# Kernel tuning notes

Hardware: AMD Instinct MI355X
Metric: run time of the kernel (lower is better)

## Reference

```python
import jax, jax.numpy as jnp
import numpy as np

NEG_SLOPE = 0.2


def setup_inputs() -> dict:
    key = jax.random.key(0)
    k1, k2, k3 = jax.random.split(key, 3)
    bs, n_agents, input_dim = 32, 512, 128
    n_heads, hidden_dim = 8, 64
    h = jax.random.normal(k1, (bs, n_agents, input_dim), dtype=jnp.float32)
    # Linear(input_dim, n_heads*hidden_dim, bias=False), stored as [in, out]
    W = jax.random.normal(k2, (input_dim, n_heads * hidden_dim), dtype=jnp.float32) * (1.0 / np.sqrt(input_dim))
    # xavier_uniform with gain=1.414 on shape (1, n_heads, 2*hidden_dim)
    fan = n_heads + 2 * hidden_dim
    bound = 1.414 * np.sqrt(6.0 / fan)
    att_a = jax.random.uniform(k3, (1, n_heads, 2 * hidden_dim), dtype=jnp.float32,
                               minval=-bound, maxval=bound)
    return {"h": h, "W": W, "att_a": att_a}


def reference(h, W, att_a):
    bs, n_agents, _ = h.shape
    n_heads = att_a.shape[1]
    hidden_dim = att_a.shape[2] // 2
    # h_prime: [bs, n_heads, n_agents, hidden_dim]
    h_prime = (h @ W).reshape(bs, n_agents, n_heads, hidden_dim).transpose(0, 2, 1, 3)
    # Additive score decomposes exactly: (a1.h_i + a2.h_j) == sum(cat(h_i,h_j)*a)
    a_src = att_a[0, :, :hidden_dim]   # [n_heads, hidden_dim]
    a_dst = att_a[0, :, hidden_dim:]   # [n_heads, hidden_dim]
    e_src = jnp.einsum('bhnd,hd->bhn', h_prime, a_src)  # score contribution of node i (row)
    e_dst = jnp.einsum('bhnd,hd->bhn', h_prime, a_dst)  # contribution of node j (col)
    e = e_src[:, :, :, None] + e_dst[:, :, None, :]     # [bs, n_heads, n, n]
    e = jnp.where(e >= 0, e, NEG_SLOPE * e)             # leaky_relu(0.2)
    attention = jax.nn.softmax(e, axis=-1)
    h_new = jnp.einsum('bhnm,bhmd->bhnd', attention, h_prime)
    return jax.nn.elu(h_new)
```

## Files before the change

### kernel.cpp

```cpp
#include <hip/hip_runtime.h>

#define BS 32
#define NA 512
#define ID 128
#define NH 8
#define HD 64
#define NHD 512
#define NEG 0.2f
#define NC 32
#define CH 16
#define NW 8
#define BPAD 136

typedef short bf16x8 __attribute__((ext_vector_type(8)));
typedef float f32x4 __attribute__((ext_vector_type(4)));

__device__ inline unsigned f2bf_bits(float x) {
  unsigned u = __float_as_uint(x);
  return (u + 0x7FFFu + ((u >> 16) & 1u)) >> 16;
}

__device__ inline void split8(const float4& x, const float4& y,
                              bf16x8& hi, bf16x8& lo) {
  float f[8] = {x.x, x.y, x.z, x.w, y.x, y.y, y.z, y.w};
  #pragma unroll
  for (int j = 0; j < 8; ++j) {
    unsigned hb = f2bf_bits(f[j]);
    float r = f[j] - __uint_as_float(hb << 16);
    unsigned lb = f2bf_bits(r);
    hi[j] = (short)hb;
    lo[j] = (short)lb;
  }
}

__global__ __launch_bounds__(256, 4) void k1_mfma(
    const float* __restrict__ h, const float* __restrict__ W,
    const float* __restrict__ att, float* __restrict__ io,
    float* __restrict__ sG, float* __restrict__ tG) {
  __shared__ unsigned short Bhi[64 * BPAD];
  __shared__ unsigned short Blo[64 * BPAD];

  int blk = blockIdx.x;
  int mt = blk >> 3;
  int n0 = (blk & 7) * 64;
  int m0 = mt * 128;
  int b = mt >> 2;
  int nbase = (mt & 3) * 128;
  int head = n0 >> 6;
  int t = threadIdx.x;
  int lane = t & 63, w = t >> 6;
  int q = lane >> 4, ml = lane & 15;

  {
    int c = t & 63, kq = t >> 6;
    const float* wsrc = W + (size_t)kq * 32 * NHD + n0 + c;
    #pragma unroll 4
    for (int kk = 0; kk < 32; ++kk) {
      int k = kq * 32 + kk;
      float x = wsrc[(size_t)kk * NHD];
      unsigned hb = f2bf_bits(x);
      float r = x - __uint_as_float(hb << 16);
      Bhi[c * BPAD + k] = (unsigned short)hb;
      Blo[c * BPAD + k] = (unsigned short)f2bf_bits(r);
    }
  }
  __syncthreads();

  f32x4 acc[2][4];
  #pragma unroll
  for (int mf = 0; mf < 2; ++mf)
    #pragma unroll
    for (int nf = 0; nf < 4; ++nf)
      acc[mf][nf] = (f32x4){0.f, 0.f, 0.f, 0.f};

  const float* A0 = h + (size_t)(m0 + w * 32 + ml) * ID;

  #pragma unroll
  for (int ks = 0; ks < 4; ++ks) {
    int ko = ks * 32 + q * 8;
    bf16x8 ah[2], al[2];
    #pragma unroll
    for (int mf = 0; mf < 2; ++mf) {
      const float* ap = A0 + mf * 16 * ID + ko;
      float4 f0 = *(const float4*)ap;
      float4 f1 = *(const float4*)(ap + 4);
      split8(f0, f1, ah[mf], al[mf]);
    }
    #pragma unroll
    for (int nf = 0; nf < 4; ++nf) {
      int bo = (nf * 16 + ml) * BPAD + ko;
      bf16x8 bh = *(const bf16x8*)&Bhi[bo];
      bf16x8 bl = *(const bf16x8*)&Blo[bo];
      #pragma unroll
      for (int mf = 0; mf < 2; ++mf) {
        acc[mf][nf] = __builtin_amdgcn_mfma_f32_16x16x32_bf16(ah[mf], bh, acc[mf][nf], 0, 0, 0);
        acc[mf][nf] = __builtin_amdgcn_mfma_f32_16x16x32_bf16(ah[mf], bl, acc[mf][nf], 0, 0, 0);
        acc[mf][nf] = __builtin_amdgcn_mfma_f32_16x16x32_bf16(al[mf], bh, acc[mf][nf], 0, 0, 0);
      }
    }
  }

  {
    float* ob = io + (((size_t)b * NH + head) * NA + nbase + w * 32) * HD + ml;
    #pragma unroll
    for (int mf = 0; mf < 2; ++mf)
      #pragma unroll
      for (int nf = 0; nf < 4; ++nf)
        #pragma unroll
        for (int r = 0; r < 4; ++r)
          ob[(size_t)(mf * 16 + q * 4 + r) * HD + nf * 16] = acc[mf][nf][r];
  }

  {
    float a_s[4], a_d[4];
    #pragma unroll
    for (int nf = 0; nf < 4; ++nf) {
      a_s[nf] = att[head * 128 + nf * 16 + ml];
      a_d[nf] = att[head * 128 + 64 + nf * 16 + ml];
    }
    #pragma unroll
    for (int mf = 0; mf < 2; ++mf) {
      #pragma unroll
      for (int r = 0; r < 4; ++r) {
        float sp = 0.f, tp = 0.f;
        #pragma unroll
        for (int nf = 0; nf < 4; ++nf) {
          float c = acc[mf][nf][r];
          sp += c * a_s[nf]; tp += c * a_d[nf];
        }
        #pragma unroll
        for (int m = 1; m < 16; m <<= 1) {
          sp += __shfl_xor(sp, m, 64);
          tp += __shfl_xor(tp, m, 64);
        }
        if (ml == 0) {
          int row = nbase + w * 32 + mf * 16 + q * 4 + r;
          size_t o = ((size_t)b * NH + head) * NA + row;
          sG[o] = sp; tG[o] = tp;
        }
      }
    }
  }
}

__global__ __launch_bounds__(512, 2) void k2_fused(
    const float* __restrict__ sG, const float* __restrict__ tG,
    float* __restrict__ io) {
  __shared__ float tv[NA]; __shared__ int tpm[NA];
  __shared__ float sv[NA]; __shared__ int spm[NA];
  __shared__ float wp[NA]; __shared__ float wn[NA];
  __shared__ float rawP8[NW * 32]; __shared__ float rawN8[NW * 32];
  __shared__ float sufPc[(NW + 1) * 32]; __shared__ float preNc[(NW + 1) * 32];
  __shared__ float zps[NA + 1]; __shared__ float znp[NA + 1];
  __shared__ float szP[NC]; __shared__ float szN[NC];
  __shared__ float sufZ[NC + 1]; __shared__ float preZ[NC + 1];
  __shared__ float4 abi[NA];
  __shared__ int jsr[NA];
  __shared__ int Earr[NA];

  int blk = blockIdx.x;
  int bh = blk >> 1;
  int dbase = (blk & 1) * 32;
  int t = threadIdx.x;
  int lane = t & 63, w = t >> 6;
  float* vbase = io + (size_t)bh * NA * HD;

  float vt = tG[(size_t)bh * NA + t]; int it = t;
  float vs = sG[(size_t)bh * NA + t]; int is_ = t;

  for (int size = 2; size <= NA; size <<= 1) {
    bool dirAsc = ((t & size) == 0);
    for (int stride = size >> 1; stride > 0; stride >>= 1) {
      float pt, ps; int pit, pis;
      if (stride >= 64) {
        tv[t] = vt; tpm[t] = it; sv[t] = vs; spm[t] = is_;
        __syncthreads();
        pt = tv[t ^ stride]; pit = tpm[t ^ stride];
        ps = sv[t ^ stride]; pis = spm[t ^ stride];
        __syncthreads();
      } else {
        pt = __shfl_xor(vt, stride, 64); pit = __shfl_xor(it, stride, 64);
        ps = __shfl_xor(vs, stride, 64); pis = __shfl_xor(is_, stride, 64);
      }
      bool mn = (((t & stride) == 0) == dirAsc);
      if (mn ? (pt < vt) : (pt > vt)) { vt = pt; it = pit; }
      if (mn ? (ps < vs) : (ps > vs)) { vs = ps; is_ = pis; }
    }
  }
  tv[t] = vt; tpm[t] = it; sv[t] = vs; spm[t] = is_;
  __syncthreads();

  float cmax = fmaxf(tv[NA - 1], 0.f);
  float amax = fmaxf(sv[NA - 1], 0.f);
  wp[t] = __expf(vt - cmax);
  wn[t] = __expf(NEG * vt - cmax);
  __syncthreads();

  float vreg[64];
  if (lane < 32) {
    float aP = 0.f, aN = 0.f;
    #pragma unroll 4
    for (int jj = 0; jj < 64; ++jj) {
      int j = (w << 6) + jj;
      float vv = vbase[(size_t)tpm[j] * HD + dbase + lane];
      vreg[jj] = vv;
      aP += wp[j] * vv;
      aN += wn[j] * vv;
    }
    rawP8[w * 32 + lane] = aP;
    rawN8[w * 32 + lane] = aN;
  }
  __syncthreads();

  if (t < 32) {
    int d = t; float run = 0.f;
    sufPc[NW * 32 + d] = 0.f;
    for (int ww = NW - 1; ww >= 0; --ww) {
      run += rawP8[ww * 32 + d]; sufPc[ww * 32 + d] = run;
    }
  } else if (t < 64) {
    int d = t - 32; float run = 0.f;
    for (int ww = 0; ww <= NW; ++ww) {
      preNc[ww * 32 + d] = run;
      if (ww < NW) run += rawN8[ww * 32 + d];
    }
  } else if (t < 96) {
    int c = t - 64; float a = 0.f;
    for (int j = c * CH; j < c * CH + CH; ++j) a += wp[j];
    szP[c] = a;
  } else if (t < 128) {
    int c = t - 96; float a = 0.f;
    for (int j = c * CH; j < c * CH + CH; ++j) a += wn[j];
    szN[c] = a;
  }
  __syncthreads();

  if (t == 0) {
    float run = 0.f; sufZ[NC] = 0.f;
    for (int cc = NC - 1; cc >= 0; --cc) { run += szP[cc]; sufZ[cc] = run; }
  } else if (t == 1) {
    float run = 0.f;
    for (int cc = 0; cc <= NC; ++cc) { preZ[cc] = run; if (cc < NC) run += szN[cc]; }
  }
  __syncthreads();

  {
    int ch = t >> 4;
    float a = 0.f;
    for (int k = t; k < ch * CH + CH; ++k) a += wp[k];
    zps[t] = a + sufZ[ch + 1];
    float b2 = 0.f;
    for (int k = ch * CH; k < t; ++k) b2 += wn[k];
    znp[t] = preZ[ch] + b2;
    if (t == 0) { zps[NA] = 0.f; znp[NA] = preZ[NC]; }
  }
  __syncthreads();

  {
    float A = __expf(vs - amax);
    float B = __expf(NEG * vs - amax);
    float key = -vs;
    int lo = 0, hi = NA;
    while (lo < hi) { int mid = (lo + hi) >> 1; if (tv[mid] < key) lo = mid + 1; else hi = mid; }
    float den = A * zps[lo] + B * znp[lo];
    float4 qv; qv.x = A; qv.y = B; qv.z = 1.f / den; qv.w = __int_as_float(is_);
    abi[t] = qv;
    jsr[t] = lo;
  }
  __syncthreads();

  {
    int lo = 0, hi = NA;
    while (lo < hi) { int mid = (lo + hi) >> 1; if (jsr[mid] > t) lo = mid + 1; else hi = mid; }
    Earr[t] = lo;
  }
  __syncthreads();

  if (lane < 32) {
    float sufPv = sufPc[w * 32 + lane];
    float preSeedN = preNc[w * 32 + lane];
    float runN = 0.f;
    size_t obase = (size_t)bh * NA * HD + dbase + lane;
    int jb = w << 6;
    int eprev = (w == 0) ? NA : Earr[jb - 1];
    #pragma unroll 1
    for (int jj = 0; jj < 64; ++jj) {
      int j = jb + jj;
      int ecur = Earr[j];
      float preNv = preSeedN + runN;
      for (int r = ecur; r < eprev; ++r) {
        float4 qv = abi[r];
        float x = (qv.x * sufPv + qv.y * preNv) * qv.z;
        int orow = __float_as_int(qv.w);
        io[obase + (size_t)orow * HD] = x > 0.f ? x : __expf(x) - 1.f;
      }
      float vv = vreg[jj];
      sufPv -= wp[j] * vv;
      runN  += wn[j] * vv;
      eprev = ecur;
    }
    if (w == NW - 1) {
      float preNv = preSeedN + runN;
      for (int r = 0; r < eprev; ++r) {
        float4 qv = abi[r];
        float x = (qv.y * preNv) * qv.z;
        int orow = __float_as_int(qv.w);
        io[obase + (size_t)orow * HD] = x > 0.f ? x : __expf(x) - 1.f;
      }
    }
  }
}

extern "C" void kernel_launch(void* const* d_in, const int* in_sizes, int n_in,
                              void* d_out, int out_size, void* d_ws, size_t ws_size,
                              hipStream_t stream) {
  const float* h   = (const float*)d_in[0];
  const float* W   = (const float*)d_in[1];
  const float* att = (const float*)d_in[2];
  float* io = (float*)d_out;
  const size_t R = (size_t)BS * NH * NA;
  float* sG = (float*)d_ws;
  float* tG = sG + R;

  k1_mfma <<<dim3(1024),        dim3(256), 0, stream>>>(h, W, att, io, sG, tG);
  k2_fused<<<dim3(BS * NH * 2), dim3(512), 0, stream>>>(sG, tG, io);
}
```

Measured before the change: 150.0 us.

## Replace sort-based prefix-sum attention with dense MFMA attention using split-bf16 weights

The second kernel no longer sorts scores and builds prefix sums with binary searches. It now computes the full attention product densely on matrix cores. The leaky-ReLU exponent is factored into per-row A/B terms and per-column wp/wn weights, so each (i,j) element only needs a sign mask to pick between two precomputed bf16 hi/lo weight pairs. Denominators come from MFMA against a ones vector. This trades the serial, sync-heavy sort and scan path for O(n²) matrix-core work, uses a workspace buffer for h', and depends on split-bf16 precision.

```diff
diff --git a/kernel.cpp b/kernel.cpp
--- a/kernel.cpp
+++ b/kernel.cpp
@@ -7,13 +7,12 @@
 #define HD 64
 #define NHD 512
 #define NEG 0.2f
-#define NC 32
-#define CH 16
-#define NW 8
 #define BPAD 136
+#define VSTR 520
 
 typedef short bf16x8 __attribute__((ext_vector_type(8)));
 typedef float f32x4 __attribute__((ext_vector_type(4)));
+typedef int   i32x4 __attribute__((ext_vector_type(4)));
 
 __device__ inline unsigned f2bf_bits(float x) {
   unsigned u = __float_as_uint(x);
@@ -33,9 +32,13 @@
   }
 }
 
+__device__ inline unsigned selpair(float x0, float x1) {
+  return (x0 >= 0.f ? 0xFFFFu : 0u) | (x1 >= 0.f ? 0xFFFF0000u : 0u);
+}
+
 __global__ __launch_bounds__(256, 4) void k1_mfma(
     const float* __restrict__ h, const float* __restrict__ W,
-    const float* __restrict__ att, float* __restrict__ io,
+    const float* __restrict__ att, float* __restrict__ hp,
     float* __restrict__ sG, float* __restrict__ tG) {
   __shared__ unsigned short Bhi[64 * BPAD];
   __shared__ unsigned short Blo[64 * BPAD];
@@ -101,7 +104,7 @@
   }
 
   {
-    float* ob = io + (((size_t)b * NH + head) * NA + nbase + w * 32) * HD + ml;
+    float* ob = hp + (((size_t)b * NH + head) * NA + nbase + w * 32) * HD + ml;
     #pragma unroll
     for (int mf = 0; mf < 2; ++mf)
       #pragma unroll
@@ -143,169 +146,158 @@
   }
 }
 
-__global__ __launch_bounds__(512, 2) void k2_fused(
-    const float* __restrict__ sG, const float* __restrict__ tG,
-    float* __restrict__ io) {
-  __shared__ float tv[NA]; __shared__ int tpm[NA];
-  __shared__ float sv[NA]; __shared__ int spm[NA];
-  __shared__ float wp[NA]; __shared__ float wn[NA];
-  __shared__ float rawP8[NW * 32]; __shared__ float rawN8[NW * 32];
-  __shared__ float sufPc[(NW + 1) * 32]; __shared__ float preNc[(NW + 1) * 32];
-  __shared__ float zps[NA + 1]; __shared__ float znp[NA + 1];
-  __shared__ float szP[NC]; __shared__ float szN[NC];
-  __shared__ float sufZ[NC + 1]; __shared__ float preZ[NC + 1];
-  __shared__ float4 abi[NA];
-  __shared__ int jsr[NA];
-  __shared__ int Earr[NA];
-
-  int blk = blockIdx.x;
-  int bh = blk >> 1;
-  int dbase = (blk & 1) * 32;
+__global__ __launch_bounds__(512) void k2_flash(
+    const float* __restrict__ hp, const float* __restrict__ sG,
+    const float* __restrict__ tG, float* __restrict__ out) {
+  __shared__ unsigned short VTh[64 * VSTR];
+  __shared__ unsigned short VTl[64 * VSTR];
+  __shared__ uint4 wpk[256];
+  __shared__ float tS[NA]; __shared__ float sS[NA];
+  __shared__ float sA[NA]; __shared__ float sB[NA];
+  __shared__ float red[8];
+
+  int bh = blockIdx.x;
   int t = threadIdx.x;
   int lane = t & 63, w = t >> 6;
-  float* vbase = io + (size_t)bh * NA * HD;
-
-  float vt = tG[(size_t)bh * NA + t]; int it = t;
-  float vs = sG[(size_t)bh * NA + t]; int is_ = t;
-
-  for (int size = 2; size <= NA; size <<= 1) {
-    bool dirAsc = ((t & size) == 0);
-    for (int stride = size >> 1; stride > 0; stride >>= 1) {
-      float pt, ps; int pit, pis;
-      if (stride >= 64) {
-        tv[t] = vt; tpm[t] = it; sv[t] = vs; spm[t] = is_;
-        __syncthreads();
-        pt = tv[t ^ stride]; pit = tpm[t ^ stride];
-        ps = sv[t ^ stride]; pis = spm[t ^ stride];
-        __syncthreads();
-      } else {
-        pt = __shfl_xor(vt, stride, 64); pit = __shfl_xor(it, stride, 64);
-        ps = __shfl_xor(vs, stride, 64); pis = __shfl_xor(is_, stride, 64);
+  int q = lane >> 4, ml = lane & 15;
+  const float* vb = hp + (size_t)bh * NA * HD;
+
+  float tj = tG[(size_t)bh * NA + t];
+  float sj = sG[(size_t)bh * NA + t];
+  tS[t] = tj; sS[t] = sj;
+  {
+    float m = tj;
+    #pragma unroll
+    for (int d = 32; d; d >>= 1) m = fmaxf(m, __shfl_xor(m, d, 64));
+    if (lane == 0) red[w] = m;
+  }
+  __syncthreads();
+  float tmax = fmaxf(fmaxf(fmaxf(red[0], red[1]), fmaxf(red[2], red[3])),
+                     fmaxf(fmaxf(red[4], red[5]), fmaxf(red[6], red[7])));
+  {
+    float y = sj + tmax;
+    float lr = fmaxf(y, 0.2f * y);
+    sA[t] = __expf(y - lr);
+    sB[t] = __expf(0.2f * y - lr);
+  }
+  if (t < 256) {
+    float t0 = tS[2 * t], t1 = tS[2 * t + 1];
+    float wp0 = __expf(t0 - tmax), wp1 = __expf(t1 - tmax);
+    float wn0 = __expf(0.2f * (t0 - tmax)), wn1 = __expf(0.2f * (t1 - tmax));
+    unsigned h0 = f2bf_bits(wp0), h1 = f2bf_bits(wp1);
+    unsigned l0 = f2bf_bits(wp0 - __uint_as_float(h0 << 16));
+    unsigned l1 = f2bf_bits(wp1 - __uint_as_float(h1 << 16));
+    unsigned n0 = f2bf_bits(wn0), n1 = f2bf_bits(wn1);
+    unsigned m0 = f2bf_bits(wn0 - __uint_as_float(n0 << 16));
+    unsigned m1 = f2bf_bits(wn1 - __uint_as_float(n1 << 16));
+    uint4 pk;
+    pk.x = h0 | (h1 << 16); pk.y = l0 | (l1 << 16);
+    pk.z = n0 | (n1 << 16); pk.w = m0 | (m1 << 16);
+    wpk[t] = pk;
+  }
+  {
+    int d = t & 63, jb = (t >> 6) * 2;
+    #pragma unroll 4
+    for (int k = 0; k < 32; ++k) {
+      int j0 = jb + k * 16;
+      float v0 = vb[(size_t)j0 * HD + d];
+      float v1 = vb[(size_t)(j0 + 1) * HD + d];
+      unsigned h0 = f2bf_bits(v0), h1 = f2bf_bits(v1);
+      unsigned l0 = f2bf_bits(v0 - __uint_as_float(h0 << 16));
+      unsigned l1 = f2bf_bits(v1 - __uint_as_float(h1 << 16));
+      *(unsigned*)&VTh[d * VSTR + j0] = h0 | (h1 << 16);
+      *(unsigned*)&VTl[d * VSTR + j0] = l0 | (l1 << 16);
+    }
+  }
+  __syncthreads();
+
+  int ri = w * 64;
+  float sIr[4];
+  #pragma unroll
+  for (int mf = 0; mf < 4; ++mf) sIr[mf] = sS[ri + mf * 16 + ml];
+
+  f32x4 acc1[4][4], acc2[4][4], aD1[4], aD2[4];
+  #pragma unroll
+  for (int mf = 0; mf < 4; ++mf) {
+    #pragma unroll
+    for (int nf = 0; nf < 4; ++nf) {
+      acc1[mf][nf] = (f32x4){0.f, 0.f, 0.f, 0.f};
+      acc2[mf][nf] = (f32x4){0.f, 0.f, 0.f, 0.f};
+    }
+    aD1[mf] = (f32x4){0.f, 0.f, 0.f, 0.f};
+    aD2[mf] = (f32x4){0.f, 0.f, 0.f, 0.f};
+  }
+
+  bf16x8 ONESB;
+  {
+    int ov = (ml == 0) ? (int)0x3F803F80 : 0;
+    i32x4 o = {ov, ov, ov, ov};
+    ONESB = __builtin_bit_cast(bf16x8, o);
+  }
+
+  #pragma unroll 1
+  for (int ch = 0; ch < 16; ++ch) {
+    int j0q = ch * 32 + q * 8;
+    float4 tqa = *(const float4*)&tS[j0q];
+    float4 tqb = *(const float4*)&tS[j0q + 4];
+    uint4 wk0 = wpk[(j0q >> 1) + 0];
+    uint4 wk1 = wpk[(j0q >> 1) + 1];
+    uint4 wk2 = wpk[(j0q >> 1) + 2];
+    uint4 wk3 = wpk[(j0q >> 1) + 3];
+    bf16x8 vh[4], vl[4];
+    #pragma unroll
+    for (int nf = 0; nf < 4; ++nf) {
+      int dd = nf * 16 + ml;
+      vh[nf] = *(const bf16x8*)&VTh[dd * VSTR + j0q];
+      vl[nf] = *(const bf16x8*)&VTl[dd * VSTR + j0q];
+    }
+    #pragma unroll
+    for (int mf = 0; mf < 4; ++mf) {
+      float si = sIr[mf];
+      unsigned s0 = selpair(si + tqa.x, si + tqa.y);
+      unsigned s1 = selpair(si + tqa.z, si + tqa.w);
+      unsigned s2 = selpair(si + tqb.x, si + tqb.y);
+      unsigned s3 = selpair(si + tqb.z, si + tqb.w);
+      i32x4 u1h = {(int)(wk0.x & s0), (int)(wk1.x & s1), (int)(wk2.x & s2), (int)(wk3.x & s3)};
+      i32x4 u1l = {(int)(wk0.y & s0), (int)(wk1.y & s1), (int)(wk2.y & s2), (int)(wk3.y & s3)};
+      i32x4 u2h = {(int)(wk0.z & ~s0), (int)(wk1.z & ~s1), (int)(wk2.z & ~s2), (int)(wk3.z & ~s3)};
+      i32x4 u2l = {(int)(wk0.w & ~s0), (int)(wk1.w & ~s1), (int)(wk2.w & ~s2), (int)(wk3.w & ~s3)};
+      bf16x8 p1h = __builtin_bit_cast(bf16x8, u1h);
+      bf16x8 p1l = __builtin_bit_cast(bf16x8, u1l);
+      bf16x8 p2h = __builtin_bit_cast(bf16x8, u2h);
+      bf16x8 p2l = __builtin_bit_cast(bf16x8, u2l);
+      #pragma unroll
+      for (int nf = 0; nf < 4; ++nf) {
+        acc1[mf][nf] = __builtin_amdgcn_mfma_f32_16x16x32_bf16(p1h, vh[nf], acc1[mf][nf], 0, 0, 0);
+        acc1[mf][nf] = __builtin_amdgcn_mfma_f32_16x16x32_bf16(p1h, vl[nf], acc1[mf][nf], 0, 0, 0);
+        acc1[mf][nf] = __builtin_amdgcn_mfma_f32_16x16x32_bf16(p1l, vh[nf], acc1[mf][nf], 0, 0, 0);
+        acc2[mf][nf] = __builtin_amdgcn_mfma_f32_16x16x32_bf16(p2h, vh[nf], acc2[mf][nf], 0, 0, 0);
+        acc2[mf][nf] = __builtin_amdgcn_mfma_f32_16x16x32_bf16(p2h, vl[nf], acc2[mf][nf], 0, 0, 0);
+        acc2[mf][nf] = __builtin_amdgcn_mfma_f32_16x16x32_bf16(p2l, vh[nf], acc2[mf][nf], 0, 0, 0);
       }
-      bool mn = (((t & stride) == 0) == dirAsc);
-      if (mn ? (pt < vt) : (pt > vt)) { vt = pt; it = pit; }
-      if (mn ? (ps < vs) : (ps > vs)) { vs = ps; is_ = pis; }
-    }
-  }
-  tv[t] = vt; tpm[t] = it; sv[t] = vs; spm[t] = is_;
-  __syncthreads();
-
-  float cmax = fmaxf(tv[NA - 1], 0.f);
-  float amax = fmaxf(sv[NA - 1], 0.f);
-  wp[t] = __expf(vt - cmax);
-  wn[t] = __expf(NEG * vt - cmax);
-  __syncthreads();
-
-  float vreg[64];
-  if (lane < 32) {
-    float aP = 0.f, aN = 0.f;
-    #pragma unroll 4
-    for (int jj = 0; jj < 64; ++jj) {
-      int j = (w << 6) + jj;
-      float vv = vbase[(size_t)tpm[j] * HD + dbase + lane];
-      vreg[jj] = vv;
-      aP += wp[j] * vv;
-      aN += wn[j] * vv;
-    }
-    rawP8[w * 32 + lane] = aP;
-    rawN8[w * 32 + lane] = aN;
-  }
-  __syncthreads();
-
-  if (t < 32) {
-    int d = t; float run = 0.f;
-    sufPc[NW * 32 + d] = 0.f;
-    for (int ww = NW - 1; ww >= 0; --ww) {
-      run += rawP8[ww * 32 + d]; sufPc[ww * 32 + d] = run;
-    }
-  } else if (t < 64) {
-    int d = t - 32; float run = 0.f;
-    for (int ww = 0; ww <= NW; ++ww) {
-      preNc[ww * 32 + d] = run;
-      if (ww < NW) run += rawN8[ww * 32 + d];
-    }
-  } else if (t < 96) {
-    int c = t - 64; float a = 0.f;
-    for (int j = c * CH; j < c * CH + CH; ++j) a += wp[j];
-    szP[c] = a;
-  } else if (t < 128) {
-    int c = t - 96; float a = 0.f;
-    for (int j = c * CH; j < c * CH + CH; ++j) a += wn[j];
-    szN[c] = a;
-  }
-  __syncthreads();
-
-  if (t == 0) {
-    float run = 0.f; sufZ[NC] = 0.f;
-    for (int cc = NC - 1; cc >= 0; --cc) { run += szP[cc]; sufZ[cc] = run; }
-  } else if (t == 1) {
-    float run = 0.f;
-    for (int cc = 0; cc <= NC; ++cc) { preZ[cc] = run; if (cc < NC) run += szN[cc]; }
-  }
-  __syncthreads();
-
-  {
-    int ch = t >> 4;
-    float a = 0.f;
-    for (int k = t; k < ch * CH + CH; ++k) a += wp[k];
-    zps[t] = a + sufZ[ch + 1];
-    float b2 = 0.f;
-    for (int k = ch * CH; k < t; ++k) b2 += wn[k];
-    znp[t] = preZ[ch] + b2;
-    if (t == 0) { zps[NA] = 0.f; znp[NA] = preZ[NC]; }
-  }
-  __syncthreads();
-
-  {
-    float A = __expf(vs - amax);
-    float B = __expf(NEG * vs - amax);
-    float key = -vs;
-    int lo = 0, hi = NA;
-    while (lo < hi) { int mid = (lo + hi) >> 1; if (tv[mid] < key) lo = mid + 1; else hi = mid; }
-    float den = A * zps[lo] + B * znp[lo];
-    float4 qv; qv.x = A; qv.y = B; qv.z = 1.f / den; qv.w = __int_as_float(is_);
-    abi[t] = qv;
-    jsr[t] = lo;
-  }
-  __syncthreads();
-
-  {
-    int lo = 0, hi = NA;
-    while (lo < hi) { int mid = (lo + hi) >> 1; if (jsr[mid] > t) lo = mid + 1; else hi = mid; }
-    Earr[t] = lo;
-  }
-  __syncthreads();
-
-  if (lane < 32) {
-    float sufPv = sufPc[w * 32 + lane];
-    float preSeedN = preNc[w * 32 + lane];
-    float runN = 0.f;
-    size_t obase = (size_t)bh * NA * HD + dbase + lane;
-    int jb = w << 6;
-    int eprev = (w == 0) ? NA : Earr[jb - 1];
-    #pragma unroll 1
-    for (int jj = 0; jj < 64; ++jj) {
-      int j = jb + jj;
-      int ecur = Earr[j];
-      float preNv = preSeedN + runN;
-      for (int r = ecur; r < eprev; ++r) {
-        float4 qv = abi[r];
-        float x = (qv.x * sufPv + qv.y * preNv) * qv.z;
-        int orow = __float_as_int(qv.w);
-        io[obase + (size_t)orow * HD] = x > 0.f ? x : __expf(x) - 1.f;
-      }
-      float vv = vreg[jj];
-      sufPv -= wp[j] * vv;
-      runN  += wn[j] * vv;
-      eprev = ecur;
-    }
-    if (w == NW - 1) {
-      float preNv = preSeedN + runN;
-      for (int r = 0; r < eprev; ++r) {
-        float4 qv = abi[r];
-        float x = (qv.y * preNv) * qv.z;
-        int orow = __float_as_int(qv.w);
-        io[obase + (size_t)orow * HD] = x > 0.f ? x : __expf(x) - 1.f;
+      aD1[mf] = __builtin_amdgcn_mfma_f32_16x16x32_bf16(p1h, ONESB, aD1[mf], 0, 0, 0);
+      aD1[mf] = __builtin_amdgcn_mfma_f32_16x16x32_bf16(p1l, ONESB, aD1[mf], 0, 0, 0);
+      aD2[mf] = __builtin_amdgcn_mfma_f32_16x16x32_bf16(p2h, ONESB, aD2[mf], 0, 0, 0);
+      aD2[mf] = __builtin_amdgcn_mfma_f32_16x16x32_bf16(p2l, ONESB, aD2[mf], 0, 0, 0);
+    }
+  }
+
+  {
+    float* ob = out + (size_t)bh * NA * HD;
+    #pragma unroll
+    for (int mf = 0; mf < 4; ++mf) {
+      #pragma unroll
+      for (int r = 0; r < 4; ++r) {
+        float d1 = __shfl(aD1[mf][r], lane & 48, 64);
+        float d2 = __shfl(aD2[mf][r], lane & 48, 64);
+        int row = ri + mf * 16 + q * 4 + r;
+        float A = sA[row], B = sB[row];
+        float inv = 1.f / (A * d1 + B * d2);
+        #pragma unroll
+        for (int nf = 0; nf < 4; ++nf) {
+          float x = (A * acc1[mf][nf][r] + B * acc2[mf][nf][r]) * inv;
+          ob[(size_t)row * HD + nf * 16 + ml] = x > 0.f ? x : __expf(x) - 1.f;
+        }
       }
     }
   }
@@ -317,11 +309,12 @@
   const float* h   = (const float*)d_in[0];
   const float* W   = (const float*)d_in[1];
   const float* att = (const float*)d_in[2];
-  float* io = (float*)d_out;
+  float* out = (float*)d_out;
   const size_t R = (size_t)BS * NH * NA;
-  float* sG = (float*)d_ws;
+  float* hp = (float*)d_ws;
+  float* sG = hp + R * HD;
   float* tG = sG + R;
 
-  k1_mfma <<<dim3(1024),        dim3(256), 0, stream>>>(h, W, att, io, sG, tG);
-  k2_fused<<<dim3(BS * NH * 2), dim3(512), 0, stream>>>(sG, tG, io);
-}
+  k1_mfma <<<dim3(1024),    dim3(256), 0, stream>>>(h, W, att, hp, sG, tG);
+  k2_flash<<<dim3(BS * NH), dim3(512), 0, stream>>>(hp, sG, tG, out);
+}
```

Result: faster. 146.0 us (-2.6%).
